# Kernel tuning notes

Measured on AMD Instinct MI355X. Metric: run time of the kernel, lower is better.

Reference implementation:

```python
import jax, jax.numpy as jnp
import numpy as np

SIGMA = 20.0


def setup_inputs() -> dict:
    key = jax.random.key(0)
    # spike trains: [batch, time_steps, n_neurons]
    spike_trains = jax.random.uniform(key, (64, 2048, 1024), dtype=jnp.float32)
    return {"spike_trains": spike_trains}


def reference(spike_trains):
    B, T, N = spike_trains.shape
    x = jnp.arange(T, dtype=jnp.float32)
    center = T // 2
    kernel = jnp.exp(-0.5 * ((x - center) / SIGMA) ** 2)
    kernel = kernel / kernel.sum()
    # weighted reduction over time: equivalent to the nested-loop dot products
    smoothed_rates = jnp.einsum('btn,t->bn', spike_trains, kernel)  # [B, N]
    return smoothed_rates
```

## Files before the change

### kernel.cpp

```cpp
#include <hip/hip_runtime.h>


#define B_DIM 64
#define T_DIM 2048
#define N_DIM 1024
#define SIGMA 20.0f

#define TC 8
#define TSTEPS (T_DIM / TC)
#define NV 32
#define BLOCK 256

__global__ __launch_bounds__(BLOCK) void GaussianSmoother_kernel(
    const float* __restrict__ x, float* __restrict__ out) {
  __shared__ float w[T_DIM];
  __shared__ float4 part[TC][NV];
  __shared__ float wavesum[BLOCK / 64];
  __shared__ float inv_sum;

  const int tid = threadIdx.x;

  float local = 0.0f;
#pragma unroll
  for (int i = tid; i < T_DIM; i += BLOCK) {
    float d = (float)(i - T_DIM / 2) * (1.0f / SIGMA);
    float e = expf(-0.5f * d * d);
    w[i] = e;
    local += e;
  }
#pragma unroll
  for (int off = 32; off > 0; off >>= 1) local += __shfl_down(local, off);
  if ((tid & 63) == 0) wavesum[tid >> 6] = local;
  __syncthreads();
  if (tid == 0) {
    float s = 0.0f;
#pragma unroll
    for (int i = 0; i < BLOCK / 64; ++i) s += wavesum[i];
    inv_sum = 1.0f / s;
  }
  __syncthreads();

  const int n4 = tid & (NV - 1);
  const int chunk = tid >> 5;
  const int b = blockIdx.x >> 3;
  const int ng = blockIdx.x & 7;

  const float4* px = (const float4*)x +
      ((size_t)b * T_DIM + (size_t)chunk * TSTEPS) * (N_DIM / 4) +
      (size_t)(ng * NV + n4);
  const float* wp = &w[chunk * TSTEPS];

  float4 acc = make_float4(0.0f, 0.0f, 0.0f, 0.0f);
#pragma unroll 8
  for (int i = 0; i < TSTEPS; ++i) {
    float4 v = px[(size_t)i * (N_DIM / 4)];
    float wt = wp[i];
    acc.x += wt * v.x;
    acc.y += wt * v.y;
    acc.z += wt * v.z;
    acc.w += wt * v.w;
  }
  part[chunk][n4] = acc;
  __syncthreads();

  if (tid < NV) {
    float4 s = part[0][tid];
#pragma unroll
    for (int c = 1; c < TC; ++c) {
      float4 p = part[c][tid];
      s.x += p.x; s.y += p.y; s.z += p.z; s.w += p.w;
    }
    const float inv = inv_sum;
    s.x *= inv; s.y *= inv; s.z *= inv; s.w *= inv;
    ((float4*)out)[(size_t)b * (N_DIM / 4) + (size_t)(ng * NV + tid)] = s;
  }
}

extern "C" void kernel_launch(void* const* d_in, const int* in_sizes, int n_in,
                              void* d_out, int out_size, void* d_ws, size_t ws_size,
                              hipStream_t stream) {
  const float* x = (const float*)d_in[0];
  float* out = (float*)d_out;
  dim3 grid(B_DIM * (N_DIM / (NV * 4)));
  GaussianSmoother_kernel<<<grid, BLOCK, 0, stream>>>(x, out);
}
```

Baseline: 664.3 us.

## Split time reduction into two kernels with full-row coalesced loads

Replaces the single fused kernel with a two-phase reduction. Phase one splits time into 16 segments per batch, and each block reads whole contiguous rows of neurons while computing only its own slice of Gaussian weights. It writes partial sums to the workspace. Phase two sums the partials, computes the normalization, and writes the output. This doubles the block count and improves load contiguity, at the cost of an extra launch and a small workspace round-trip.

```diff
diff --git a/kernel.cpp b/kernel.cpp
--- a/kernel.cpp
+++ b/kernel.cpp
@@ -6,74 +6,71 @@
 #define N_DIM 1024
 #define SIGMA 20.0f
 
-#define TC 8
-#define TSTEPS (T_DIM / TC)
-#define NV 32
+#define S_SPLIT 16
+#define R_STEPS (T_DIM / S_SPLIT)
 #define BLOCK 256
 
-__global__ __launch_bounds__(BLOCK) void GaussianSmoother_kernel(
-    const float* __restrict__ x, float* __restrict__ out) {
-  __shared__ float w[T_DIM];
-  __shared__ float4 part[TC][NV];
+__global__ __launch_bounds__(BLOCK) void GaussianSmoother_phase1(
+    const float* __restrict__ x, float4* __restrict__ part) {
+  __shared__ float w[R_STEPS];
+
+  const int tid = threadIdx.x;
+  const int b = blockIdx.x & (B_DIM - 1);
+  const int s = blockIdx.x >> 6;
+  const int t0 = s * R_STEPS;
+
+  if (tid < R_STEPS) {
+    float d = (float)(t0 + tid - T_DIM / 2) * (1.0f / SIGMA);
+    w[tid] = expf(-0.5f * d * d);
+  }
+  __syncthreads();
+
+  const float4* px = (const float4*)x + ((size_t)b * T_DIM + t0) * (N_DIM / 4) + tid;
+
+  float4 acc = make_float4(0.0f, 0.0f, 0.0f, 0.0f);
+#pragma unroll 8
+  for (int i = 0; i < R_STEPS; ++i) {
+    float4 v = px[(size_t)i * (N_DIM / 4)];
+    float wt = w[i];
+    acc.x += wt * v.x;
+    acc.y += wt * v.y;
+    acc.z += wt * v.z;
+    acc.w += wt * v.w;
+  }
+
+  part[((size_t)s * B_DIM + b) * (N_DIM / 4) + tid] = acc;
+}
+
+__global__ __launch_bounds__(BLOCK) void GaussianSmoother_phase2(
+    const float4* __restrict__ part, float4* __restrict__ out) {
   __shared__ float wavesum[BLOCK / 64];
-  __shared__ float inv_sum;
 
   const int tid = threadIdx.x;
 
   float local = 0.0f;
 #pragma unroll
-  for (int i = tid; i < T_DIM; i += BLOCK) {
-    float d = (float)(i - T_DIM / 2) * (1.0f / SIGMA);
-    float e = expf(-0.5f * d * d);
-    w[i] = e;
-    local += e;
+  for (int t = tid; t < T_DIM; t += BLOCK) {
+    float d = (float)(t - T_DIM / 2) * (1.0f / SIGMA);
+    local += expf(-0.5f * d * d);
   }
 #pragma unroll
   for (int off = 32; off > 0; off >>= 1) local += __shfl_down(local, off);
   if ((tid & 63) == 0) wavesum[tid >> 6] = local;
   __syncthreads();
-  if (tid == 0) {
-    float s = 0.0f;
+  float s0 = 0.0f;
 #pragma unroll
-    for (int i = 0; i < BLOCK / 64; ++i) s += wavesum[i];
-    inv_sum = 1.0f / s;
+  for (int i = 0; i < BLOCK / 64; ++i) s0 += wavesum[i];
+  const float inv = 1.0f / s0;
+
+  const int b = blockIdx.x;
+  float4 acc = make_float4(0.0f, 0.0f, 0.0f, 0.0f);
+#pragma unroll
+  for (int s = 0; s < S_SPLIT; ++s) {
+    float4 v = part[((size_t)s * B_DIM + b) * (N_DIM / 4) + tid];
+    acc.x += v.x; acc.y += v.y; acc.z += v.z; acc.w += v.w;
   }
-  __syncthreads();
-
-  const int n4 = tid & (NV - 1);
-  const int chunk = tid >> 5;
-  const int b = blockIdx.x >> 3;
-  const int ng = blockIdx.x & 7;
-
-  const float4* px = (const float4*)x +
-      ((size_t)b * T_DIM + (size_t)chunk * TSTEPS) * (N_DIM / 4) +
-      (size_t)(ng * NV + n4);
-  const float* wp = &w[chunk * TSTEPS];
-
-  float4 acc = make_float4(0.0f, 0.0f, 0.0f, 0.0f);
-#pragma unroll 8
-  for (int i = 0; i < TSTEPS; ++i) {
-    float4 v = px[(size_t)i * (N_DIM / 4)];
-    float wt = wp[i];
-    acc.x += wt * v.x;
-    acc.y += wt * v.y;
-    acc.z += wt * v.z;
-    acc.w += wt * v.w;
-  }
-  part[chunk][n4] = acc;
-  __syncthreads();
-
-  if (tid < NV) {
-    float4 s = part[0][tid];
-#pragma unroll
-    for (int c = 1; c < TC; ++c) {
-      float4 p = part[c][tid];
-      s.x += p.x; s.y += p.y; s.z += p.z; s.w += p.w;
-    }
-    const float inv = inv_sum;
-    s.x *= inv; s.y *= inv; s.z *= inv; s.w *= inv;
-    ((float4*)out)[(size_t)b * (N_DIM / 4) + (size_t)(ng * NV + tid)] = s;
-  }
+  acc.x *= inv; acc.y *= inv; acc.z *= inv; acc.w *= inv;
+  out[(size_t)b * (N_DIM / 4) + tid] = acc;
 }
 
 extern "C" void kernel_launch(void* const* d_in, const int* in_sizes, int n_in,
@@ -81,6 +78,8 @@
                               hipStream_t stream) {
   const float* x = (const float*)d_in[0];
   float* out = (float*)d_out;
-  dim3 grid(B_DIM * (N_DIM / (NV * 4)));
-  GaussianSmoother_kernel<<<grid, BLOCK, 0, stream>>>(x, out);
+  float4* part = (float4*)d_ws;
+
+  GaussianSmoother_phase1<<<dim3(B_DIM * S_SPLIT), BLOCK, 0, stream>>>(x, part);
+  GaussianSmoother_phase2<<<dim3(B_DIM), BLOCK, 0, stream>>>(part, (float4*)out);
 }
```

Measured after the change: 673.6 us. Within noise of the previous version (+1.4%).
